# Optimization experiments

Measured on AMD Instinct MI355X. Metric: run time of the kernel, lower is better.

Reference implementation:

```python
import jax, jax.numpy as jnp
import numpy as np

B, L, H, F = 8, 1024, 512, 4

def setup_inputs() -> dict:
    key = jax.random.key(0)
    ks = jax.random.split(key, 5)
    x = jax.random.normal(ks[0], (B, L, H), dtype=jnp.float32)
    x_mask = jax.random.randint(ks[1], (B, L), 0, 2).astype(jnp.int32)
    W_proj = jax.random.normal(ks[2], (H, H * F), dtype=jnp.float32) * (1.0 / np.sqrt(H))
    b_proj = jnp.zeros((H * F,), dtype=jnp.float32)
    W_gate = jax.random.normal(ks[3], (2 * H, 2 * H), dtype=jnp.float32) * (1.0 / np.sqrt(2 * H))
    b_gate = jnp.zeros((2 * H,), dtype=jnp.float32)
    return {"x": x, "x_mask": x_mask, "W_proj": W_proj, "b_proj": b_proj,
            "W_gate": W_gate, "b_gate": b_gate}

def masked_softmax(logits, mask, eps=1e-13):
    # allennlp-style masked softmax used throughout sgnlp:
    # softmax(logits * mask) * mask, renormalized.
    m = mask.astype(logits.dtype)
    p = jax.nn.softmax(logits * m, axis=-1) * m
    return p / (p.sum(axis=-1, keepdims=True) + eps)

def reference(x, x_mask, W_proj, b_proj, W_gate, b_gate):
    b, l, h = x.shape
    # multi-factor projection: (B,L,H) -> (B,L,H,F) with relu (Linear activation='relu', dropout=0)
    y = jax.nn.relu(jnp.einsum('blh,hk->blk', x, W_proj) + b_proj)
    y = y.reshape(b, l, h, F)
    # per-factor self-attn scores stacked on last axis: (B,L,L,F)
    scores = jnp.einsum('blhf,bmhf->blmf', y, y)
    self_attn = scores.max(axis=-1)  # attn_pooling == 'max'
    # pairwise mask, zero diagonal
    mask = x_mask[:, :, None] * x_mask[:, None, :]
    mask = mask * (1 - jnp.eye(l, dtype=mask.dtype))
    alpha = masked_softmax(self_attn, mask)
    multi_attn_enc = jnp.einsum('blm,bmh->blh', alpha, x)
    joint = jnp.concatenate([x, multi_attn_enc], axis=-1)  # (B,L,2H)
    gate = jax.nn.sigmoid(jnp.einsum('blk,kj->blj', joint, W_gate) + b_gate)
    return gate * joint
```

## Files before the change

kernel.cpp:

```cpp
#include <hip/hip_runtime.h>


typedef _Float16 half8 __attribute__((ext_vector_type(8)));
typedef _Float16 half4 __attribute__((ext_vector_type(4)));
typedef float floatx4 __attribute__((ext_vector_type(4)));

typedef const __attribute__((address_space(1))) void* gas_ptr;
typedef __attribute__((address_space(3))) void* las_ptr;


template<int NCH, int NT>
__device__ __forceinline__ void init_ptrs(const _Float16* src, int row0, int ld,
                                          const _Float16* gp[NCH]) {
  int t = threadIdx.x;
#pragma unroll
  for (int p = 0; p < NCH; ++p) {
    int c = p * NT + t;
    int row = c >> 3;
    int kg = c & 7;
    int gk = (kg ^ (row & 7)) << 3;
    gp[p] = src + (size_t)(row0 + row) * ld + gk;
  }
}

template<int NCH, int NT>
__device__ __forceinline__ void stage(const _Float16* const gp[NCH], _Float16* ldsbuf) {
  int t = threadIdx.x;
#pragma unroll
  for (int p = 0; p < NCH; ++p)
    __builtin_amdgcn_global_load_lds((gas_ptr)gp[p],
                                     (las_ptr)(ldsbuf + t * 8 + p * NT * 8), 16, 0, 0);
}

template<int NCH>
__device__ __forceinline__ void bump(const _Float16* gp[NCH], int d) {
#pragma unroll
  for (int p = 0; p < NCH; ++p) gp[p] += d;
}

__device__ __forceinline__ half8 frag_ld(const _Float16* lds, int row, int g) {
  return *(const half8*)(lds + row * 64 + ((g ^ (row & 7)) << 3));
}


__global__ void x_prep_kernel(const float* __restrict__ in, _Float16* __restrict__ x16,
                              _Float16* __restrict__ xT) {
  __shared__ float tile[32][33];
  const int R = 1024, C = 512;
  int c0 = blockIdx.x * 32, r0 = blockIdx.y * 32;
  size_t boff = (size_t)blockIdx.z * R * C;
  in += boff; x16 += boff; xT += boff;
  int tx = threadIdx.x & 31, ty = threadIdx.x >> 5;
#pragma unroll
  for (int i = 0; i < 32; i += 8) {
    float v = in[(size_t)(r0 + ty + i) * C + c0 + tx];
    tile[ty + i][tx] = v;
    x16[(size_t)(r0 + ty + i) * C + c0 + tx] = (_Float16)v;
  }
  __syncthreads();
#pragma unroll
  for (int i = 0; i < 32; i += 8)
    xT[(size_t)(c0 + ty + i) * R + r0 + tx] = (_Float16)tile[tx][ty + i];
}

__global__ void w_prep_kernel(const float* __restrict__ Wp, _Float16* __restrict__ WpT,
                              const float* __restrict__ Wg, _Float16* __restrict__ WgT) {
  __shared__ float tile[32][33];
  const float* in; _Float16* out; int R, C, c0, r0;
  if (blockIdx.z == 0) {
    in = Wp; out = WpT; R = 512; C = 2048;
    c0 = blockIdx.x * 32; r0 = blockIdx.y * 32;
  } else {
    in = Wg; out = WgT; R = 1024; C = 1024;
    c0 = (blockIdx.x & 31) * 32; r0 = (blockIdx.y * 2 + (blockIdx.x >> 5)) * 32;
  }
  int tx = threadIdx.x & 31, ty = threadIdx.x >> 5;
#pragma unroll
  for (int i = 0; i < 32; i += 8)
    tile[ty + i][tx] = in[(size_t)(r0 + ty + i) * C + c0 + tx];
  __syncthreads();
#pragma unroll
  for (int i = 0; i < 32; i += 8)
    out[(size_t)(c0 + ty + i) * R + r0 + tx] = (_Float16)tile[tx][ty + i];
}


__device__ __forceinline__ void mfma_tile44(const _Float16* lds_a, const _Float16* lds_b,
                                            floatx4 acc[4][4], int wm, int wn,
                                            int l16, int quad) {
#pragma unroll
  for (int kf = 0; kf < 2; ++kf) {
    half8 af[4], bf[4];
#pragma unroll
    for (int i = 0; i < 4; ++i) af[i] = frag_ld(lds_a, wm * 64 + i * 16 + l16, kf * 4 + quad);
#pragma unroll
    for (int i = 0; i < 4; ++i) bf[i] = frag_ld(lds_b, wn * 64 + i * 16 + l16, kf * 4 + quad);
#pragma unroll
    for (int mi = 0; mi < 4; ++mi)
#pragma unroll
      for (int ni = 0; ni < 4; ++ni)
        acc[mi][ni] = __builtin_amdgcn_mfma_f32_16x16x32_f16(af[mi], bf[ni], acc[mi][ni], 0, 0, 0);
  }
}

#define ZERO_ACC44(acc)                                 \
  _Pragma("unroll") for (int mi = 0; mi < 4; ++mi)      \
  _Pragma("unroll") for (int ni = 0; ni < 4; ++ni)      \
  _Pragma("unroll") for (int r = 0; r < 4; ++r) acc[mi][ni][r] = 0.0f;

__global__ __launch_bounds__(256) void proj_kernel(const _Float16* __restrict__ x16,
                                                   const _Float16* __restrict__ WpT,
                                                   const float* __restrict__ bp,
                                                   _Float16* __restrict__ y_t) {
  __shared__ __align__(16) _Float16 ldsA[2][128 * 64];
  __shared__ __align__(16) _Float16 ldsB[2][128 * 64];
  int i0 = blockIdx.x * 128, n0 = blockIdx.y * 128;
  int t = threadIdx.x, lane = t & 63, w = t >> 6;
  int wm = w >> 1, wn = w & 1, quad = lane >> 4, l16 = lane & 15;
  const _Float16* gpA[4]; const _Float16* gpB[4];
  init_ptrs<4, 256>(x16, i0, 512, gpA);
  init_ptrs<4, 256>(WpT, n0, 512, gpB);
  floatx4 acc[4][4];
  ZERO_ACC44(acc);
  stage<4, 256>(gpA, ldsA[0]); bump<4>(gpA, 64);
  stage<4, 256>(gpB, ldsB[0]); bump<4>(gpB, 64);
#pragma unroll 1
  for (int kt = 0; kt < 8; ++kt) {
    __syncthreads();
    if (kt < 7) {
      stage<4, 256>(gpA, ldsA[(kt + 1) & 1]); bump<4>(gpA, 64);
      stage<4, 256>(gpB, ldsB[(kt + 1) & 1]); bump<4>(gpB, 64);
    }
    mfma_tile44(ldsA[kt & 1], ldsB[kt & 1], acc, wm, wn, l16, quad);
  }
#pragma unroll
  for (int mi = 0; mi < 4; ++mi)
#pragma unroll
    for (int ni = 0; ni < 4; ++ni)
#pragma unroll
      for (int r = 0; r < 4; ++r) {
        int gr = i0 + wm * 64 + mi * 16 + quad * 4 + r;
        int gc = n0 + wn * 64 + ni * 16 + l16;
        float c = fmaxf(acc[mi][ni][r] + bp[gc], 0.0f);
        int b = gr >> 10, l = gr & 1023;
        int f = gc & 3, h = gc >> 2;
        y_t[(((size_t)(b * 4 + f)) * 1024 + l) * 512 + h] = (_Float16)c;
      }
}


__global__ __launch_bounds__(512, 4) void score_kernel(const _Float16* __restrict__ y_t,
                                                       float* __restrict__ S) {
  __shared__ __align__(16) _Float16 ldsA[2][128 * 64];
  __shared__ __align__(16) _Float16 ldsB[2][128 * 64];
  int id = blockIdx.x;
  int b = id & 7;
  int tile = id >> 3;
  int i0 = (tile >> 3) * 128, j0 = (tile & 7) * 128;
  int t = threadIdx.x, lane = t & 63, w = t >> 6;
  int wm = w >> 2, wn = w & 3, quad = lane >> 4, l16 = lane & 15;
  const int PLANE = 1024 * 512;
  const _Float16* base = y_t + (size_t)b * 4 * PLANE;
  const _Float16* gpA[2]; const _Float16* gpB[2];
  init_ptrs<2, 512>(base, i0, 512, gpA);
  init_ptrs<2, 512>(base, j0, 512, gpB);
  floatx4 acc[4][2], smax[4][2];
#pragma unroll
  for (int mi = 0; mi < 4; ++mi)
#pragma unroll
    for (int ni = 0; ni < 2; ++ni)
#pragma unroll
      for (int r = 0; r < 4; ++r) acc[mi][ni][r] = 0.0f;
  stage<2, 512>(gpA, ldsA[0]); bump<2>(gpA, 64);
  stage<2, 512>(gpB, ldsB[0]); bump<2>(gpB, 64);
#pragma unroll 1
  for (int f = 0; f < 4; ++f) {
#pragma unroll 1
    for (int kt = 0; kt < 8; ++kt) {
      __syncthreads();
      if (f * 8 + kt < 31) {
        if (kt == 7) { bump<2>(gpA, PLANE - 512); bump<2>(gpB, PLANE - 512); }
        stage<2, 512>(gpA, ldsA[(kt + 1) & 1]); bump<2>(gpA, 64);
        stage<2, 512>(gpB, ldsB[(kt + 1) & 1]); bump<2>(gpB, 64);
      }
      const _Float16* la = ldsA[kt & 1];
      const _Float16* lb = ldsB[kt & 1];
#pragma unroll
      for (int kf = 0; kf < 2; ++kf) {
        half8 af[4], bf[2];
#pragma unroll
        for (int i = 0; i < 4; ++i) af[i] = frag_ld(la, wm * 64 + i * 16 + l16, kf * 4 + quad);
#pragma unroll
        for (int i = 0; i < 2; ++i) bf[i] = frag_ld(lb, wn * 32 + i * 16 + l16, kf * 4 + quad);
#pragma unroll
        for (int mi = 0; mi < 4; ++mi)
#pragma unroll
          for (int ni = 0; ni < 2; ++ni)
            acc[mi][ni] = __builtin_amdgcn_mfma_f32_16x16x32_f16(af[mi], bf[ni], acc[mi][ni], 0, 0, 0);
      }
    }
    if (f == 0) {
#pragma unroll
      for (int mi = 0; mi < 4; ++mi)
#pragma unroll
        for (int ni = 0; ni < 2; ++ni) smax[mi][ni] = acc[mi][ni];
    } else {
#pragma unroll
      for (int mi = 0; mi < 4; ++mi)
#pragma unroll
        for (int ni = 0; ni < 2; ++ni)
#pragma unroll
          for (int r = 0; r < 4; ++r)
            smax[mi][ni][r] = fmaxf(smax[mi][ni][r], acc[mi][ni][r]);
    }
#pragma unroll
    for (int mi = 0; mi < 4; ++mi)
#pragma unroll
      for (int ni = 0; ni < 2; ++ni)
#pragma unroll
        for (int r = 0; r < 4; ++r) acc[mi][ni][r] = 0.0f;
  }
  float* Sb = S + (size_t)b * 1024 * 1024;
#pragma unroll
  for (int mi = 0; mi < 4; ++mi)
#pragma unroll
    for (int ni = 0; ni < 2; ++ni)
#pragma unroll
      for (int r = 0; r < 4; ++r) {
        int gi = i0 + wm * 64 + mi * 16 + quad * 4 + r;
        int gj = j0 + wn * 32 + ni * 16 + l16;
        Sb[(size_t)gi * 1024 + gj] = smax[mi][ni][r];
      }
}


__global__ __launch_bounds__(256) void softmax_kernel(const float* __restrict__ S,
                                                      const int* __restrict__ xmask,
                                                      _Float16* __restrict__ alpha) {
  __shared__ float red[16];
  int row = blockIdx.x;
  int b = row >> 10, l = row & 1023;
  const float* sr = S + (size_t)row * 1024;
  const int* mr = xmask + b * 1024;
  int t = threadIdx.x, lane = t & 63, wid = t >> 6;
  int rm = mr[l];
  float v[4], mm[4];
  float vmax = 0.0f;
#pragma unroll
  for (int q = 0; q < 4; ++q) {
    int i = t + q * 256;
    int m = (rm && mr[i] && (i != l)) ? 1 : 0;
    mm[q] = (float)m;
    v[q] = m ? sr[i] : 0.0f;
    vmax = fmaxf(vmax, v[q]);
  }
  for (int off = 32; off; off >>= 1) vmax = fmaxf(vmax, __shfl_down(vmax, off));
  if (lane == 0) red[wid] = vmax;
  __syncthreads();
  if (t == 0) red[8] = fmaxf(fmaxf(red[0], red[1]), fmaxf(red[2], red[3]));
  __syncthreads();
  vmax = red[8];
  float e[4], E = 0.0f, E2 = 0.0f;
#pragma unroll
  for (int q = 0; q < 4; ++q) {
    e[q] = expf(v[q] - vmax);
    E += e[q];
    E2 += e[q] * mm[q];
  }
  for (int off = 32; off; off >>= 1) {
    E += __shfl_down(E, off);
    E2 += __shfl_down(E2, off);
  }
  if (lane == 0) { red[wid] = E; red[4 + wid] = E2; }
  __syncthreads();
  if (t == 0) {
    red[9] = red[0] + red[1] + red[2] + red[3];
    red[10] = red[4] + red[5] + red[6] + red[7];
  }
  __syncthreads();
  E = red[9]; E2 = red[10];
  float inv = 1.0f / (E2 + 1e-13f * E);
  _Float16* ar = alpha + (size_t)row * 1024;
#pragma unroll
  for (int q = 0; q < 4; ++q) {
    int i = t + q * 256;
    ar[i] = (_Float16)(e[q] * mm[q] * inv);
  }
}


__global__ __launch_bounds__(256) void attn_kernel(const _Float16* __restrict__ alpha,
                                                   const _Float16* __restrict__ xT,
                                                   _Float16* __restrict__ enc) {
  __shared__ __align__(16) _Float16 ldsA[2][64 * 64];
  __shared__ __align__(16) _Float16 ldsB[2][128 * 64];
  int id = blockIdx.x;
  int b = id & 7;
  int r2 = id >> 3;
  int i0 = (r2 >> 2) * 64;
  int n0 = (r2 & 3) * 128;
  const _Float16* A = alpha + (size_t)b * 1024 * 1024;
  const _Float16* Bm = xT + (size_t)b * 512 * 1024;
  int t = threadIdx.x, lane = t & 63, wn = t >> 6;
  int quad = lane >> 4, l16 = lane & 15;
  const _Float16* gpA[2]; const _Float16* gpB[4];
  init_ptrs<2, 256>(A, i0, 1024, gpA);
  init_ptrs<4, 256>(Bm, n0, 1024, gpB);
  floatx4 acc[4][2];
#pragma unroll
  for (int mi = 0; mi < 4; ++mi)
#pragma unroll
    for (int ni = 0; ni < 2; ++ni)
#pragma unroll
      for (int r = 0; r < 4; ++r) acc[mi][ni][r] = 0.0f;
  stage<2, 256>(gpA, ldsA[0]); bump<2>(gpA, 64);
  stage<4, 256>(gpB, ldsB[0]); bump<4>(gpB, 64);
#pragma unroll 1
  for (int kt = 0; kt < 16; ++kt) {
    __syncthreads();
    if (kt < 15) {
      stage<2, 256>(gpA, ldsA[(kt + 1) & 1]); bump<2>(gpA, 64);
      stage<4, 256>(gpB, ldsB[(kt + 1) & 1]); bump<4>(gpB, 64);
    }
    const _Float16* la = ldsA[kt & 1];
    const _Float16* lb = ldsB[kt & 1];
#pragma unroll
    for (int kf = 0; kf < 2; ++kf) {
      half8 af[4], bf[2];
#pragma unroll
      for (int i = 0; i < 4; ++i) af[i] = frag_ld(la, i * 16 + l16, kf * 4 + quad);
#pragma unroll
      for (int i = 0; i < 2; ++i) bf[i] = frag_ld(lb, wn * 32 + i * 16 + l16, kf * 4 + quad);
#pragma unroll
      for (int mi = 0; mi < 4; ++mi)
#pragma unroll
        for (int ni = 0; ni < 2; ++ni)
          acc[mi][ni] = __builtin_amdgcn_mfma_f32_16x16x32_f16(af[mi], bf[ni], acc[mi][ni], 0, 0, 0);
    }
  }
  _Float16* eb = enc + (size_t)b * 1024 * 512;
#pragma unroll
  for (int mi = 0; mi < 4; ++mi)
#pragma unroll
    for (int ni = 0; ni < 2; ++ni)
#pragma unroll
      for (int r = 0; r < 4; ++r) {
        int gr = i0 + mi * 16 + quad * 4 + r;
        int gc = n0 + wn * 32 + ni * 16 + l16;
        eb[(size_t)gr * 512 + gc] = (_Float16)acc[mi][ni][r];
      }
}


__global__ __launch_bounds__(256) void gate_kernel(const _Float16* __restrict__ x16,
                                                   const _Float16* __restrict__ enc,
                                                   const _Float16* __restrict__ WgT,
                                                   const float* __restrict__ bg,
                                                   float* __restrict__ out) {
  __shared__ __align__(16) _Float16 ldsA[2][128 * 64];
  __shared__ __align__(16) _Float16 ldsB[2][128 * 64];
  int i0 = blockIdx.x * 128, n0 = blockIdx.y * 128;
  int t = threadIdx.x, lane = t & 63, w = t >> 6;
  int wm = w >> 1, wn = w & 1, quad = lane >> 4, l16 = lane & 15;
  const _Float16* gpA[4]; const _Float16* gpA2[4]; const _Float16* gpB[4];
  init_ptrs<4, 256>(x16, i0, 512, gpA);
  init_ptrs<4, 256>(enc, i0, 512, gpA2);
  init_ptrs<4, 256>(WgT, n0, 1024, gpB);
  floatx4 acc[4][4];
  ZERO_ACC44(acc);
  stage<4, 256>(gpA, ldsA[0]); bump<4>(gpA, 64);
  stage<4, 256>(gpB, ldsB[0]); bump<4>(gpB, 64);
#pragma unroll 1
  for (int kt = 0; kt < 16; ++kt) {
    __syncthreads();
    if (kt < 15) {
      if (kt < 7) { stage<4, 256>(gpA,  ldsA[(kt + 1) & 1]); bump<4>(gpA, 64); }
      else        { stage<4, 256>(gpA2, ldsA[(kt + 1) & 1]); bump<4>(gpA2, 64); }
      stage<4, 256>(gpB, ldsB[(kt + 1) & 1]); bump<4>(gpB, 64);
    }
    mfma_tile44(ldsA[kt & 1], ldsB[kt & 1], acc, wm, wn, l16, quad);
  }
#pragma unroll
  for (int mi = 0; mi < 4; ++mi)
#pragma unroll
    for (int ni = 0; ni < 4; ++ni)
#pragma unroll
      for (int r = 0; r < 4; ++r) {
        int gr = i0 + wm * 64 + mi * 16 + quad * 4 + r;
        int gc = n0 + wn * 64 + ni * 16 + l16;
        float c = acc[mi][ni][r] + bg[gc];
        float g = 1.0f / (1.0f + expf(-c));
        float jv = (gc < 512) ? (float)x16[(size_t)gr * 512 + gc]
                              : (float)enc[(size_t)gr * 512 + (gc - 512)];
        out[(size_t)gr * 1024 + gc] = g * jv;
      }
}


extern "C" void kernel_launch(void* const* d_in, const int* in_sizes, int n_in,
                              void* d_out, int out_size, void* d_ws, size_t ws_size,
                              hipStream_t stream) {
  const float* x  = (const float*)d_in[0];
  const int* xm   = (const int*)d_in[1];
  const float* Wp = (const float*)d_in[2];
  const float* bp = (const float*)d_in[3];
  const float* Wg = (const float*)d_in[4];
  const float* bg = (const float*)d_in[5];
  float* out = (float*)d_out;

  char* ws = (char*)d_ws;
  const size_t MB = 1024 * 1024;
  _Float16* x16 = (_Float16*)(ws);
  _Float16* xT  = (_Float16*)(ws + 8 * MB);
  _Float16* WpT = (_Float16*)(ws + 16 * MB);
  _Float16* WgT = (_Float16*)(ws + 18 * MB);
  _Float16* y_t = (_Float16*)(ws + 20 * MB);
  float*    S   = (float*)(ws + 52 * MB);
  _Float16* alpha = (_Float16*)(ws + 20 * MB);
  _Float16* enc   = (_Float16*)(ws + 36 * MB);

  x_prep_kernel<<<dim3(16, 32, 8), 256, 0, stream>>>(x, x16, xT);
  w_prep_kernel<<<dim3(64, 16, 2), 256, 0, stream>>>(Wp, WpT, Wg, WgT);

  proj_kernel<<<dim3(64, 16), 256, 0, stream>>>(x16, WpT, bp, y_t);
  score_kernel<<<512, 512, 0, stream>>>(y_t, S);
  softmax_kernel<<<8192, 256, 0, stream>>>(S, xm, alpha);
  attn_kernel<<<512, 256, 0, stream>>>(alpha, xT, enc);
  gate_kernel<<<dim3(64, 8), 256, 0, stream>>>(x16, enc, WgT, bg, out);
}
```

Baseline: 220.1 us.

## Exploit score symmetry to compute upper-triangle tiles and widen GEMM blocks to 512 threads

The score matrix y·yᵀ is symmetric, so the score kernel now computes only upper-triangular 128x128 tiles (36 per batch instead of 64). Each off-diagonal tile is written transposed through a padded LDS buffer to fill the mirror block, which removes nearly half of the score MFMA work and y loads. The proj and gate kernels are also changed to 512-thread blocks with a 4x2 per-wave accumulator layout, reusing the score kernel's tiling. In exchange the mirrored store adds an extra write pass and more synchronisation, and the smaller per-wave tiles lower register reuse in proj and gate.

```diff
diff --git a/kernel.cpp b/kernel.cpp
--- a/kernel.cpp
+++ b/kernel.cpp
@@ -2,7 +2,6 @@
 
 
 typedef _Float16 half8 __attribute__((ext_vector_type(8)));
-typedef _Float16 half4 __attribute__((ext_vector_type(4)));
 typedef float floatx4 __attribute__((ext_vector_type(4)));
 
 typedef const __attribute__((address_space(1))) void* gas_ptr;
@@ -41,6 +40,29 @@
 __device__ __forceinline__ half8 frag_ld(const _Float16* lds, int row, int g) {
   return *(const half8*)(lds + row * 64 + ((g ^ (row & 7)) << 3));
 }
+
+__device__ __forceinline__ void mfma_tile42(const _Float16* la, const _Float16* lb,
+                                            floatx4 acc[4][2], int wm, int wn,
+                                            int l16, int quad) {
+#pragma unroll
+  for (int kf = 0; kf < 2; ++kf) {
+    half8 af[4], bf[2];
+#pragma unroll
+    for (int i = 0; i < 4; ++i) af[i] = frag_ld(la, wm * 64 + i * 16 + l16, kf * 4 + quad);
+#pragma unroll
+    for (int i = 0; i < 2; ++i) bf[i] = frag_ld(lb, wn * 32 + i * 16 + l16, kf * 4 + quad);
+#pragma unroll
+    for (int mi = 0; mi < 4; ++mi)
+#pragma unroll
+      for (int ni = 0; ni < 2; ++ni)
+        acc[mi][ni] = __builtin_amdgcn_mfma_f32_16x16x32_f16(af[mi], bf[ni], acc[mi][ni], 0, 0, 0);
+  }
+}
+
+#define ZERO_ACC42(acc)                                 \
+  _Pragma("unroll") for (int mi = 0; mi < 4; ++mi)      \
+  _Pragma("unroll") for (int ni = 0; ni < 2; ++ni)      \
+  _Pragma("unroll") for (int r = 0; r < 4; ++r) acc[mi][ni][r] = 0.0f;
 
 
 __global__ void x_prep_kernel(const float* __restrict__ in, _Float16* __restrict__ x16,
@@ -85,62 +107,39 @@
 }
 
 
-__device__ __forceinline__ void mfma_tile44(const _Float16* lds_a, const _Float16* lds_b,
-                                            floatx4 acc[4][4], int wm, int wn,
-                                            int l16, int quad) {
-#pragma unroll
-  for (int kf = 0; kf < 2; ++kf) {
-    half8 af[4], bf[4];
-#pragma unroll
-    for (int i = 0; i < 4; ++i) af[i] = frag_ld(lds_a, wm * 64 + i * 16 + l16, kf * 4 + quad);
-#pragma unroll
-    for (int i = 0; i < 4; ++i) bf[i] = frag_ld(lds_b, wn * 64 + i * 16 + l16, kf * 4 + quad);
-#pragma unroll
-    for (int mi = 0; mi < 4; ++mi)
-#pragma unroll
-      for (int ni = 0; ni < 4; ++ni)
-        acc[mi][ni] = __builtin_amdgcn_mfma_f32_16x16x32_f16(af[mi], bf[ni], acc[mi][ni], 0, 0, 0);
-  }
-}
-
-#define ZERO_ACC44(acc)                                 \
-  _Pragma("unroll") for (int mi = 0; mi < 4; ++mi)      \
-  _Pragma("unroll") for (int ni = 0; ni < 4; ++ni)      \
-  _Pragma("unroll") for (int r = 0; r < 4; ++r) acc[mi][ni][r] = 0.0f;
-
-__global__ __launch_bounds__(256) void proj_kernel(const _Float16* __restrict__ x16,
-                                                   const _Float16* __restrict__ WpT,
-                                                   const float* __restrict__ bp,
-                                                   _Float16* __restrict__ y_t) {
+__global__ __launch_bounds__(512, 4) void proj_kernel(const _Float16* __restrict__ x16,
+                                                      const _Float16* __restrict__ WpT,
+                                                      const float* __restrict__ bp,
+                                                      _Float16* __restrict__ y_t) {
   __shared__ __align__(16) _Float16 ldsA[2][128 * 64];
   __shared__ __align__(16) _Float16 ldsB[2][128 * 64];
   int i0 = blockIdx.x * 128, n0 = blockIdx.y * 128;
   int t = threadIdx.x, lane = t & 63, w = t >> 6;
-  int wm = w >> 1, wn = w & 1, quad = lane >> 4, l16 = lane & 15;
-  const _Float16* gpA[4]; const _Float16* gpB[4];
-  init_ptrs<4, 256>(x16, i0, 512, gpA);
-  init_ptrs<4, 256>(WpT, n0, 512, gpB);
-  floatx4 acc[4][4];
-  ZERO_ACC44(acc);
-  stage<4, 256>(gpA, ldsA[0]); bump<4>(gpA, 64);
-  stage<4, 256>(gpB, ldsB[0]); bump<4>(gpB, 64);
+  int wm = w >> 2, wn = w & 3, quad = lane >> 4, l16 = lane & 15;
+  const _Float16* gpA[2]; const _Float16* gpB[2];
+  init_ptrs<2, 512>(x16, i0, 512, gpA);
+  init_ptrs<2, 512>(WpT, n0, 512, gpB);
+  floatx4 acc[4][2];
+  ZERO_ACC42(acc);
+  stage<2, 512>(gpA, ldsA[0]); bump<2>(gpA, 64);
+  stage<2, 512>(gpB, ldsB[0]); bump<2>(gpB, 64);
 #pragma unroll 1
   for (int kt = 0; kt < 8; ++kt) {
     __syncthreads();
     if (kt < 7) {
-      stage<4, 256>(gpA, ldsA[(kt + 1) & 1]); bump<4>(gpA, 64);
-      stage<4, 256>(gpB, ldsB[(kt + 1) & 1]); bump<4>(gpB, 64);
-    }
-    mfma_tile44(ldsA[kt & 1], ldsB[kt & 1], acc, wm, wn, l16, quad);
+      stage<2, 512>(gpA, ldsA[(kt + 1) & 1]); bump<2>(gpA, 64);
+      stage<2, 512>(gpB, ldsB[(kt + 1) & 1]); bump<2>(gpB, 64);
+    }
+    mfma_tile42(ldsA[kt & 1], ldsB[kt & 1], acc, wm, wn, l16, quad);
   }
 #pragma unroll
   for (int mi = 0; mi < 4; ++mi)
 #pragma unroll
-    for (int ni = 0; ni < 4; ++ni)
+    for (int ni = 0; ni < 2; ++ni)
 #pragma unroll
       for (int r = 0; r < 4; ++r) {
         int gr = i0 + wm * 64 + mi * 16 + quad * 4 + r;
-        int gc = n0 + wn * 64 + ni * 16 + l16;
+        int gc = n0 + wn * 32 + ni * 16 + l16;
         float c = fmaxf(acc[mi][ni][r] + bp[gc], 0.0f);
         int b = gr >> 10, l = gr & 1023;
         int f = gc & 3, h = gc >> 2;
@@ -151,12 +150,18 @@
 
 __global__ __launch_bounds__(512, 4) void score_kernel(const _Float16* __restrict__ y_t,
                                                        float* __restrict__ S) {
-  __shared__ __align__(16) _Float16 ldsA[2][128 * 64];
-  __shared__ __align__(16) _Float16 ldsB[2][128 * 64];
+  __shared__ __align__(16) char smem[128 * 129 * 4];
+  _Float16* LA0 = (_Float16*)smem;
+  _Float16* LA1 = (_Float16*)(smem + 16384);
+  _Float16* LB0 = (_Float16*)(smem + 32768);
+  _Float16* LB1 = (_Float16*)(smem + 49152);
   int id = blockIdx.x;
   int b = id & 7;
-  int tile = id >> 3;
-  int i0 = (tile >> 3) * 128, j0 = (tile & 7) * 128;
+  int tt = id >> 3;
+  int ti = 0;
+  while (tt >= 8 - ti) { tt -= 8 - ti; ++ti; }
+  int tj = ti + tt;
+  int i0 = ti * 128, j0 = tj * 128;
   int t = threadIdx.x, lane = t & 63, w = t >> 6;
   int wm = w >> 2, wn = w & 3, quad = lane >> 4, l16 = lane & 15;
   const int PLANE = 1024 * 512;
@@ -165,14 +170,9 @@
   init_ptrs<2, 512>(base, i0, 512, gpA);
   init_ptrs<2, 512>(base, j0, 512, gpB);
   floatx4 acc[4][2], smax[4][2];
-#pragma unroll
-  for (int mi = 0; mi < 4; ++mi)
-#pragma unroll
-    for (int ni = 0; ni < 2; ++ni)
-#pragma unroll
-      for (int r = 0; r < 4; ++r) acc[mi][ni][r] = 0.0f;
-  stage<2, 512>(gpA, ldsA[0]); bump<2>(gpA, 64);
-  stage<2, 512>(gpB, ldsB[0]); bump<2>(gpB, 64);
+  ZERO_ACC42(acc);
+  stage<2, 512>(gpA, LA0); bump<2>(gpA, 64);
+  stage<2, 512>(gpB, LB0); bump<2>(gpB, 64);
 #pragma unroll 1
   for (int f = 0; f < 4; ++f) {
 #pragma unroll 1
@@ -180,24 +180,10 @@
       __syncthreads();
       if (f * 8 + kt < 31) {
         if (kt == 7) { bump<2>(gpA, PLANE - 512); bump<2>(gpB, PLANE - 512); }
-        stage<2, 512>(gpA, ldsA[(kt + 1) & 1]); bump<2>(gpA, 64);
-        stage<2, 512>(gpB, ldsB[(kt + 1) & 1]); bump<2>(gpB, 64);
+        stage<2, 512>(gpA, ((kt + 1) & 1) ? LA1 : LA0); bump<2>(gpA, 64);
+        stage<2, 512>(gpB, ((kt + 1) & 1) ? LB1 : LB0); bump<2>(gpB, 64);
       }
-      const _Float16* la = ldsA[kt & 1];
-      const _Float16* lb = ldsB[kt & 1];
-#pragma unroll
-      for (int kf = 0; kf < 2; ++kf) {
-        half8 af[4], bf[2];
-#pragma unroll
-        for (int i = 0; i < 4; ++i) af[i] = frag_ld(la, wm * 64 + i * 16 + l16, kf * 4 + quad);
-#pragma unroll
-        for (int i = 0; i < 2; ++i) bf[i] = frag_ld(lb, wn * 32 + i * 16 + l16, kf * 4 + quad);
-#pragma unroll
-        for (int mi = 0; mi < 4; ++mi)
-#pragma unroll
-          for (int ni = 0; ni < 2; ++ni)
-            acc[mi][ni] = __builtin_amdgcn_mfma_f32_16x16x32_f16(af[mi], bf[ni], acc[mi][ni], 0, 0, 0);
-      }
+      mfma_tile42((kt & 1) ? LA1 : LA0, (kt & 1) ? LB1 : LB0, acc, wm, wn, l16, quad);
     }
     if (f == 0) {
 #pragma unroll
@@ -213,12 +199,7 @@
           for (int r = 0; r < 4; ++r)
             smax[mi][ni][r] = fmaxf(smax[mi][ni][r], acc[mi][ni][r]);
     }
-#pragma unroll
-    for (int mi = 0; mi < 4; ++mi)
-#pragma unroll
-      for (int ni = 0; ni < 2; ++ni)
-#pragma unroll
-        for (int r = 0; r < 4; ++r) acc[mi][ni][r] = 0.0f;
+    ZERO_ACC42(acc);
   }
   float* Sb = S + (size_t)b * 1024 * 1024;
 #pragma unroll
@@ -231,6 +212,25 @@
         int gj = j0 + wn * 32 + ni * 16 + l16;
         Sb[(size_t)gi * 1024 + gj] = smax[mi][ni][r];
       }
+  if (ti != tj) {
+    __syncthreads();
+    float* tl = (float*)smem;
+#pragma unroll
+    for (int mi = 0; mi < 4; ++mi)
+#pragma unroll
+      for (int ni = 0; ni < 2; ++ni)
+#pragma unroll
+        for (int r = 0; r < 4; ++r)
+          tl[(wm * 64 + mi * 16 + quad * 4 + r) * 129 + (wn * 32 + ni * 16 + l16)] =
+              smax[mi][ni][r];
+    __syncthreads();
+#pragma unroll 1
+    for (int k = 0; k < 32; ++k) {
+      int flat = k * 512 + t;
+      int rm = flat >> 7, cm = flat & 127;
+      Sb[(size_t)(j0 + rm) * 1024 + (i0 + cm)] = tl[cm * 129 + rm];
+    }
+  }
 }
 
 
@@ -307,12 +307,7 @@
   init_ptrs<2, 256>(A, i0, 1024, gpA);
   init_ptrs<4, 256>(Bm, n0, 1024, gpB);
   floatx4 acc[4][2];
-#pragma unroll
-  for (int mi = 0; mi < 4; ++mi)
-#pragma unroll
-    for (int ni = 0; ni < 2; ++ni)
-#pragma unroll
-      for (int r = 0; r < 4; ++r) acc[mi][ni][r] = 0.0f;
+  ZERO_ACC42(acc);
   stage<2, 256>(gpA, ldsA[0]); bump<2>(gpA, 64);
   stage<4, 256>(gpB, ldsB[0]); bump<4>(gpB, 64);
 #pragma unroll 1
@@ -352,42 +347,42 @@
 }
 
 
-__global__ __launch_bounds__(256) void gate_kernel(const _Float16* __restrict__ x16,
-                                                   const _Float16* __restrict__ enc,
-                                                   const _Float16* __restrict__ WgT,
-                                                   const float* __restrict__ bg,
-                                                   float* __restrict__ out) {
+__global__ __launch_bounds__(512, 4) void gate_kernel(const _Float16* __restrict__ x16,
+                                                      const _Float16* __restrict__ enc,
+                                                      const _Float16* __restrict__ WgT,
+                                                      const float* __restrict__ bg,
+                                                      float* __restrict__ out) {
   __shared__ __align__(16) _Float16 ldsA[2][128 * 64];
   __shared__ __align__(16) _Float16 ldsB[2][128 * 64];
   int i0 = blockIdx.x * 128, n0 = blockIdx.y * 128;
   int t = threadIdx.x, lane = t & 63, w = t >> 6;
-  int wm = w >> 1, wn = w & 1, quad = lane >> 4, l16 = lane & 15;
-  const _Float16* gpA[4]; const _Float16* gpA2[4]; const _Float16* gpB[4];
-  init_ptrs<4, 256>(x16, i0, 512, gpA);
-  init_ptrs<4, 256>(enc, i0, 512, gpA2);
-  init_ptrs<4, 256>(WgT, n0, 1024, gpB);
-  floatx4 acc[4][4];
-  ZERO_ACC44(acc);
-  stage<4, 256>(gpA, ldsA[0]); bump<4>(gpA, 64);
-  stage<4, 256>(gpB, ldsB[0]); bump<4>(gpB, 64);
+  int wm = w >> 2, wn = w & 3, quad = lane >> 4, l16 = lane & 15;
+  const _Float16* gpA[2]; const _Float16* gpA2[2]; const _Float16* gpB[2];
+  init_ptrs<2, 512>(x16, i0, 512, gpA);
+  init_ptrs<2, 512>(enc, i0, 512, gpA2);
+  init_ptrs<2, 512>(WgT, n0, 1024, gpB);
+  floatx4 acc[4][2];
+  ZERO_ACC42(acc);
+  stage<2, 512>(gpA, ldsA[0]); bump<2>(gpA, 64);
+  stage<2, 512>(gpB, ldsB[0]); bump<2>(gpB, 64);
 #pragma unroll 1
   for (int kt = 0; kt < 16; ++kt) {
     __syncthreads();
     if (kt < 15) {
-      if (kt < 7) { stage<4, 256>(gpA,  ldsA[(kt + 1) & 1]); bump<4>(gpA, 64); }
-      else        { stage<4, 256>(gpA2, ldsA[(kt + 1) & 1]); bump<4>(gpA2, 64); }
-      stage<4, 256>(gpB, ldsB[(kt + 1) & 1]); bump<4>(gpB, 64);
-    }
-    mfma_tile44(ldsA[kt & 1], ldsB[kt & 1], acc, wm, wn, l16, quad);
+      if (kt < 7) { stage<2, 512>(gpA,  ldsA[(kt + 1) & 1]); bump<2>(gpA, 64); }
+      else        { stage<2, 512>(gpA2, ldsA[(kt + 1) & 1]); bump<2>(gpA2, 64); }
+      stage<2, 512>(gpB, ldsB[(kt + 1) & 1]); bump<2>(gpB, 64);
+    }
+    mfma_tile42(ldsA[kt & 1], ldsB[kt & 1], acc, wm, wn, l16, quad);
   }
 #pragma unroll
   for (int mi = 0; mi < 4; ++mi)
 #pragma unroll
-    for (int ni = 0; ni < 4; ++ni)
+    for (int ni = 0; ni < 2; ++ni)
 #pragma unroll
       for (int r = 0; r < 4; ++r) {
         int gr = i0 + wm * 64 + mi * 16 + quad * 4 + r;
-        int gc = n0 + wn * 64 + ni * 16 + l16;
+        int gc = n0 + wn * 32 + ni * 16 + l16;
         float c = acc[mi][ni][r] + bg[gc];
         float g = 1.0f / (1.0f + expf(-c));
         float jv = (gc < 512) ? (float)x16[(size_t)gr * 512 + gc]
@@ -422,9 +417,9 @@
   x_prep_kernel<<<dim3(16, 32, 8), 256, 0, stream>>>(x, x16, xT);
   w_prep_kernel<<<dim3(64, 16, 2), 256, 0, stream>>>(Wp, WpT, Wg, WgT);
 
-  proj_kernel<<<dim3(64, 16), 256, 0, stream>>>(x16, WpT, bp, y_t);
-  score_kernel<<<512, 512, 0, stream>>>(y_t, S);
+  proj_kernel<<<dim3(64, 16), 512, 0, stream>>>(x16, WpT, bp, y_t);
+  score_kernel<<<288, 512, 0, stream>>>(y_t, S);
   softmax_kernel<<<8192, 256, 0, stream>>>(S, xm, alpha);
   attn_kernel<<<512, 256, 0, stream>>>(alpha, xT, enc);
-  gate_kernel<<<dim3(64, 8), 256, 0, stream>>>(x16, enc, WgT, bg, out);
-}
+  gate_kernel<<<dim3(64, 8), 512, 0, stream>>>(x16, enc, WgT, bg, out);
+}
```

Result: no change. 217.2 us (-1.3%).

## Exploit score matrix symmetry: compute upper-triangular tiles and mirror via LDS transpose

Applied to the files above, without the earlier changes.

The per-factor score matrix y·yᵀ is symmetric, and so is its max over factors, so the score kernel now computes only the upper-triangular 128x128 tiles (36 per batch instead of 64). Each off-diagonal tile is written once directly and once transposed through a padded LDS buffer. This cuts the score GEMM work nearly in half. In exchange the grid has fewer blocks, off-diagonal blocks do an extra transposed store pass with stride-1024 writes, and the shared-memory footprint grows to hold the padded float tile.

```diff
diff --git a/kernel.cpp b/kernel.cpp
--- a/kernel.cpp
+++ b/kernel.cpp
@@ -2,7 +2,6 @@
 
 
 typedef _Float16 half8 __attribute__((ext_vector_type(8)));
-typedef _Float16 half4 __attribute__((ext_vector_type(4)));
 typedef float floatx4 __attribute__((ext_vector_type(4)));
 
 typedef const __attribute__((address_space(1))) void* gas_ptr;
@@ -41,6 +40,52 @@
 __device__ __forceinline__ half8 frag_ld(const _Float16* lds, int row, int g) {
   return *(const half8*)(lds + row * 64 + ((g ^ (row & 7)) << 3));
 }
+
+__device__ __forceinline__ void mfma_tile44(const _Float16* lds_a, const _Float16* lds_b,
+                                            floatx4 acc[4][4], int wm, int wn,
+                                            int l16, int quad) {
+#pragma unroll
+  for (int kf = 0; kf < 2; ++kf) {
+    half8 af[4], bf[4];
+#pragma unroll
+    for (int i = 0; i < 4; ++i) af[i] = frag_ld(lds_a, wm * 64 + i * 16 + l16, kf * 4 + quad);
+#pragma unroll
+    for (int i = 0; i < 4; ++i) bf[i] = frag_ld(lds_b, wn * 64 + i * 16 + l16, kf * 4 + quad);
+#pragma unroll
+    for (int mi = 0; mi < 4; ++mi)
+#pragma unroll
+      for (int ni = 0; ni < 4; ++ni)
+        acc[mi][ni] = __builtin_amdgcn_mfma_f32_16x16x32_f16(af[mi], bf[ni], acc[mi][ni], 0, 0, 0);
+  }
+}
+
+#define ZERO_ACC44(acc)                                 \
+  _Pragma("unroll") for (int mi = 0; mi < 4; ++mi)      \
+  _Pragma("unroll") for (int ni = 0; ni < 4; ++ni)      \
+  _Pragma("unroll") for (int r = 0; r < 4; ++r) acc[mi][ni][r] = 0.0f;
+
+__device__ __forceinline__ void mfma_tile42(const _Float16* la, const _Float16* lb,
+                                            floatx4 acc[4][2], int wm, int wn,
+                                            int l16, int quad) {
+#pragma unroll
+  for (int kf = 0; kf < 2; ++kf) {
+    half8 af[4], bf[2];
+#pragma unroll
+    for (int i = 0; i < 4; ++i) af[i] = frag_ld(la, wm * 64 + i * 16 + l16, kf * 4 + quad);
+#pragma unroll
+    for (int i = 0; i < 2; ++i) bf[i] = frag_ld(lb, wn * 32 + i * 16 + l16, kf * 4 + quad);
+#pragma unroll
+    for (int mi = 0; mi < 4; ++mi)
+#pragma unroll
+      for (int ni = 0; ni < 2; ++ni)
+        acc[mi][ni] = __builtin_amdgcn_mfma_f32_16x16x32_f16(af[mi], bf[ni], acc[mi][ni], 0, 0, 0);
+  }
+}
+
+#define ZERO_ACC42(acc)                                 \
+  _Pragma("unroll") for (int mi = 0; mi < 4; ++mi)      \
+  _Pragma("unroll") for (int ni = 0; ni < 2; ++ni)      \
+  _Pragma("unroll") for (int r = 0; r < 4; ++r) acc[mi][ni][r] = 0.0f;
 
 
 __global__ void x_prep_kernel(const float* __restrict__ in, _Float16* __restrict__ x16,
@@ -84,29 +129,6 @@
     out[(size_t)(c0 + ty + i) * R + r0 + tx] = (_Float16)tile[tx][ty + i];
 }
 
-
-__device__ __forceinline__ void mfma_tile44(const _Float16* lds_a, const _Float16* lds_b,
-                                            floatx4 acc[4][4], int wm, int wn,
-                                            int l16, int quad) {
-#pragma unroll
-  for (int kf = 0; kf < 2; ++kf) {
-    half8 af[4], bf[4];
-#pragma unroll
-    for (int i = 0; i < 4; ++i) af[i] = frag_ld(lds_a, wm * 64 + i * 16 + l16, kf * 4 + quad);
-#pragma unroll
-    for (int i = 0; i < 4; ++i) bf[i] = frag_ld(lds_b, wn * 64 + i * 16 + l16, kf * 4 + quad);
-#pragma unroll
-    for (int mi = 0; mi < 4; ++mi)
-#pragma unroll
-      for (int ni = 0; ni < 4; ++ni)
-        acc[mi][ni] = __builtin_amdgcn_mfma_f32_16x16x32_f16(af[mi], bf[ni], acc[mi][ni], 0, 0, 0);
-  }
-}
-
-#define ZERO_ACC44(acc)                                 \
-  _Pragma("unroll") for (int mi = 0; mi < 4; ++mi)      \
-  _Pragma("unroll") for (int ni = 0; ni < 4; ++ni)      \
-  _Pragma("unroll") for (int r = 0; r < 4; ++r) acc[mi][ni][r] = 0.0f;
 
 __global__ __launch_bounds__(256) void proj_kernel(const _Float16* __restrict__ x16,
                                                    const _Float16* __restrict__ WpT,
@@ -151,12 +173,18 @@
 
 __global__ __launch_bounds__(512, 4) void score_kernel(const _Float16* __restrict__ y_t,
                                                        float* __restrict__ S) {
-  __shared__ __align__(16) _Float16 ldsA[2][128 * 64];
-  __shared__ __align__(16) _Float16 ldsB[2][128 * 64];
+  __shared__ __align__(16) char smem[128 * 129 * 4];
+  _Float16* LA0 = (_Float16*)smem;
+  _Float16* LA1 = (_Float16*)(smem + 16384);
+  _Float16* LB0 = (_Float16*)(smem + 32768);
+  _Float16* LB1 = (_Float16*)(smem + 49152);
   int id = blockIdx.x;
   int b = id & 7;
-  int tile = id >> 3;
-  int i0 = (tile >> 3) * 128, j0 = (tile & 7) * 128;
+  int tt = id >> 3;
+  int ti = 0;
+  while (tt >= 8 - ti) { tt -= 8 - ti; ++ti; }
+  int tj = ti + tt;
+  int i0 = ti * 128, j0 = tj * 128;
   int t = threadIdx.x, lane = t & 63, w = t >> 6;
   int wm = w >> 2, wn = w & 3, quad = lane >> 4, l16 = lane & 15;
   const int PLANE = 1024 * 512;
@@ -165,14 +193,9 @@
   init_ptrs<2, 512>(base, i0, 512, gpA);
   init_ptrs<2, 512>(base, j0, 512, gpB);
   floatx4 acc[4][2], smax[4][2];
-#pragma unroll
-  for (int mi = 0; mi < 4; ++mi)
-#pragma unroll
-    for (int ni = 0; ni < 2; ++ni)
-#pragma unroll
-      for (int r = 0; r < 4; ++r) acc[mi][ni][r] = 0.0f;
-  stage<2, 512>(gpA, ldsA[0]); bump<2>(gpA, 64);
-  stage<2, 512>(gpB, ldsB[0]); bump<2>(gpB, 64);
+  ZERO_ACC42(acc);
+  stage<2, 512>(gpA, LA0); bump<2>(gpA, 64);
+  stage<2, 512>(gpB, LB0); bump<2>(gpB, 64);
 #pragma unroll 1
   for (int f = 0; f < 4; ++f) {
 #pragma unroll 1
@@ -180,24 +203,10 @@
       __syncthreads();
       if (f * 8 + kt < 31) {
         if (kt == 7) { bump<2>(gpA, PLANE - 512); bump<2>(gpB, PLANE - 512); }
-        stage<2, 512>(gpA, ldsA[(kt + 1) & 1]); bump<2>(gpA, 64);
-        stage<2, 512>(gpB, ldsB[(kt + 1) & 1]); bump<2>(gpB, 64);
+        stage<2, 512>(gpA, ((kt + 1) & 1) ? LA1 : LA0); bump<2>(gpA, 64);
+        stage<2, 512>(gpB, ((kt + 1) & 1) ? LB1 : LB0); bump<2>(gpB, 64);
       }
-      const _Float16* la = ldsA[kt & 1];
-      const _Float16* lb = ldsB[kt & 1];
-#pragma unroll
-      for (int kf = 0; kf < 2; ++kf) {
-        half8 af[4], bf[2];
-#pragma unroll
-        for (int i = 0; i < 4; ++i) af[i] = frag_ld(la, wm * 64 + i * 16 + l16, kf * 4 + quad);
-#pragma unroll
-        for (int i = 0; i < 2; ++i) bf[i] = frag_ld(lb, wn * 32 + i * 16 + l16, kf * 4 + quad);
-#pragma unroll
-        for (int mi = 0; mi < 4; ++mi)
-#pragma unroll
-          for (int ni = 0; ni < 2; ++ni)
-            acc[mi][ni] = __builtin_amdgcn_mfma_f32_16x16x32_f16(af[mi], bf[ni], acc[mi][ni], 0, 0, 0);
-      }
+      mfma_tile42((kt & 1) ? LA1 : LA0, (kt & 1) ? LB1 : LB0, acc, wm, wn, l16, quad);
     }
     if (f == 0) {
 #pragma unroll
@@ -213,12 +222,7 @@
           for (int r = 0; r < 4; ++r)
             smax[mi][ni][r] = fmaxf(smax[mi][ni][r], acc[mi][ni][r]);
     }
-#pragma unroll
-    for (int mi = 0; mi < 4; ++mi)
-#pragma unroll
-      for (int ni = 0; ni < 2; ++ni)
-#pragma unroll
-        for (int r = 0; r < 4; ++r) acc[mi][ni][r] = 0.0f;
+    ZERO_ACC42(acc);
   }
   float* Sb = S + (size_t)b * 1024 * 1024;
 #pragma unroll
@@ -231,6 +235,25 @@
         int gj = j0 + wn * 32 + ni * 16 + l16;
         Sb[(size_t)gi * 1024 + gj] = smax[mi][ni][r];
       }
+  if (ti != tj) {
+    __syncthreads();
+    float* tl = (float*)smem;
+#pragma unroll
+    for (int mi = 0; mi < 4; ++mi)
+#pragma unroll
+      for (int ni = 0; ni < 2; ++ni)
+#pragma unroll
+        for (int r = 0; r < 4; ++r)
+          tl[(wm * 64 + mi * 16 + quad * 4 + r) * 129 + (wn * 32 + ni * 16 + l16)] =
+              smax[mi][ni][r];
+    __syncthreads();
+#pragma unroll 1
+    for (int k = 0; k < 32; ++k) {
+      int flat = k * 512 + t;
+      int rm = flat >> 7, cm = flat & 127;
+      Sb[(size_t)(j0 + rm) * 1024 + (i0 + cm)] = tl[cm * 129 + rm];
+    }
+  }
 }
 
 
@@ -307,12 +330,7 @@
   init_ptrs<2, 256>(A, i0, 1024, gpA);
   init_ptrs<4, 256>(Bm, n0, 1024, gpB);
   floatx4 acc[4][2];
-#pragma unroll
-  for (int mi = 0; mi < 4; ++mi)
-#pragma unroll
-    for (int ni = 0; ni < 2; ++ni)
-#pragma unroll
-      for (int r = 0; r < 4; ++r) acc[mi][ni][r] = 0.0f;
+  ZERO_ACC42(acc);
   stage<2, 256>(gpA, ldsA[0]); bump<2>(gpA, 64);
   stage<4, 256>(gpB, ldsB[0]); bump<4>(gpB, 64);
 #pragma unroll 1
@@ -423,7 +441,7 @@
   w_prep_kernel<<<dim3(64, 16, 2), 256, 0, stream>>>(Wp, WpT, Wg, WgT);
 
   proj_kernel<<<dim3(64, 16), 256, 0, stream>>>(x16, WpT, bp, y_t);
-  score_kernel<<<512, 512, 0, stream>>>(y_t, S);
+  score_kernel<<<288, 512, 0, stream>>>(y_t, S);
   softmax_kernel<<<8192, 256, 0, stream>>>(S, xm, alpha);
   attn_kernel<<<512, 256, 0, stream>>>(alpha, xT, enc);
   gate_kernel<<<dim3(64, 8), 256, 0, stream>>>(x16, enc, WgT, bg, out);
```

New measurement: 216.9 us. No clear change (-1.5%).
